# Kernel tuning notes

Measured on AMD Instinct MI355X. Metric: run time of the kernel, lower is better.

The kernel has to match this reference:

```python
import jax, jax.numpy as jnp
import numpy as np

N = 100000   # active voxels (stride=1 -> output coords == input coords)
C_IN = 64
C_OUT = 64
K3 = 27      # 3x3x3 kernel offsets
M = 40000    # rulebook pairs per kernel offset
EPS = 1e-5


def setup_inputs() -> dict:
    key = jax.random.key(0)
    k1, k2, k3, k4 = jax.random.split(key, 4)
    x = jax.random.normal(k1, (N, C_IN), dtype=jnp.float32)
    # conv weights per kernel offset: [K3, inc, outc]
    W = jax.random.normal(k2, (K3, C_IN, C_OUT), dtype=jnp.float32) * 0.05
    gamma = jnp.ones((C_OUT,), dtype=jnp.float32)
    beta = jnp.zeros((C_OUT,), dtype=jnp.float32)
    # rulebook: for each offset k, M (input_idx, output_idx) pairs
    in_idx = jax.random.randint(k3, (K3, M), 0, N, dtype=jnp.int32)
    out_idx = jax.random.randint(k4, (K3, M), 0, N, dtype=jnp.int32)
    return {"x": x, "W": W, "gamma": gamma, "beta": beta,
            "in_idx": in_idx, "out_idx": out_idx}


def reference(x, W, gamma, beta, in_idx, out_idx):
    n_out = x.shape[0]  # stride=1: output voxel set == input voxel set
    # gather: [K3, M, C_IN]
    feat = x[in_idx]
    # batched GEMM over kernel offsets: [K3, M, C_OUT]
    contrib = jnp.einsum('kmi,kio->kmo', feat, W)
    # scatter-add into output voxels
    out = jnp.zeros((n_out, W.shape[2]), dtype=x.dtype)
    out = out.at[out_idx.reshape(-1)].add(contrib.reshape(-1, W.shape[2]))
    # BatchNorm over active points (training-mode batch stats, biased var)
    mean = jnp.mean(out, axis=0)
    var = jnp.mean(jnp.square(out - mean), axis=0)
    y = (out - mean) * jax.lax.rsqrt(var + EPS) * gamma + beta
    # ReLU
    return jnp.maximum(y, 0.0)
```

## Files before the change

### kernel.cpp

```cpp
#include <hip/hip_runtime.h>


#define N_VOX   100000
#define NPAD    100096
#define K3      27
#define M_PAIRS 40000
#define NPAIRS  (K3 * M_PAIRS)
#define BN_EPS  1e-5f
#define NBINS   (K3 * NPAD)
#define AUXMAX  172032
#define AUXCAP  (AUXMAX - 1)
#define ZROW    (N_VOX + AUXMAX - 1)

#define OFF_WT     0u
#define OFF_STATS  221184u
#define OFF_CTRS   221696u
#define OFF_BT     221760u
#define OFF_NODE   11032128u
#define OFF_LIST   19672128u
#define OFF_XB     20360320u
#define OFF_BH     (OFF_XB + (size_t)N_VOX * 128u)
#define WS_NEED    ((size_t)OFF_XB + (size_t)(N_VOX + AUXMAX) * 128u)

#define NB_WT    432
#define NB_XB    3125
#define NB_BUILD 4219
#define GRID_IB  (NB_WT + NB_XB + 1 + NB_BUILD)

typedef __attribute__((ext_vector_type(8))) short bf16x8;
typedef __attribute__((ext_vector_type(4))) float f32x4;

__device__ __forceinline__ short f2bf(float f) {
  unsigned u = __builtin_bit_cast(unsigned, f);
  u += 0x7FFFu + ((u >> 16) & 1u);
  return (short)(u >> 16);
}
__device__ __forceinline__ float bf2f(short s) {
  unsigned u = ((unsigned)(unsigned short)s) << 16;
  return __builtin_bit_cast(float, u);
}

__global__ __launch_bounds__(256) void init_build_kernel(const float* __restrict__ W,
                                                         const float* __restrict__ x,
                                                         const int* __restrict__ in_idx,
                                                         const int* __restrict__ out_idx,
                                                         short* __restrict__ wt,
                                                         short* __restrict__ xb,
                                                         int* __restrict__ bh,
                                                         int2* __restrict__ node) {
  int b = blockIdx.x, t = threadIdx.x;
  if (b < NB_WT) {
    int id = b * 256 + t;
    int k = id >> 12, rem = id & 4095, c = rem >> 6, i = rem & 63;
    wt[id] = f2bf(W[(k << 12) + (i << 6) + c]);
  } else if (b < NB_WT + NB_XB) {
    int id = (b - NB_WT) * 256 + t;
    if (id < N_VOX * 8) {
      float4 lo = ((const float4*)x)[id * 2];
      float4 hi = ((const float4*)x)[id * 2 + 1];
      bf16x8 v;
      v[0] = f2bf(lo.x); v[1] = f2bf(lo.y); v[2] = f2bf(lo.z); v[3] = f2bf(lo.w);
      v[4] = f2bf(hi.x); v[5] = f2bf(hi.y); v[6] = f2bf(hi.z); v[7] = f2bf(hi.w);
      ((bf16x8*)xb)[id] = v;
    }
  } else if (b == NB_WT + NB_XB) {
    if (t < 8) {
      bf16x8 z = {0, 0, 0, 0, 0, 0, 0, 0};
      ((bf16x8*)(xb + (size_t)ZROW * 64))[t] = z;
    }
  } else {
    int id = (b - (NB_WT + NB_XB + 1)) * 256 + t;
    if (id < NPAIRS) {
      int k  = id / M_PAIRS;
      int in = in_idx[id];
      int o  = out_idx[id];
      int bb = k * NPAD + o;
      int old = atomicExch(&bh[bb], id);
      node[id] = make_int2(old, in);
    }
  }
}

__global__ __launch_bounds__(256) void compact_kernel(const int* __restrict__ bh,
                                                      const int2* __restrict__ node,
                                                      int* __restrict__ bt,
                                                      int* __restrict__ list,
                                                      int* __restrict__ ctrs) {
  __shared__ int l_cnt, l_base;
  int t = threadIdx.x;
  if (t == 0) l_cnt = 0;
  __syncthreads();
  int w = blockIdx.x * 256 + t;
  bool ok = (w < NBINS / 4);
  int4 h4 = ok ? ((const int4*)bh)[w] : make_int4(-1, -1, -1, -1);
  int hv[4] = {h4.x, h4.y, h4.z, h4.w};
  int gv[4], lp[4];
  int2 n0[4];
  #pragma unroll
  for (int s = 0; s < 4; ++s) {
    lp[s] = -1;
    if (hv[s] < 0) { gv[s] = ZROW; }
    else {
      n0[s] = node[hv[s]];
      if (n0[s].x < 0) gv[s] = n0[s].y;
      else             lp[s] = atomicAdd(&l_cnt, 1);
    }
  }
  __syncthreads();
  if (t == 0) l_base = (l_cnt > 0) ? atomicAdd(&ctrs[0], l_cnt) : 0;
  __syncthreads();
  #pragma unroll
  for (int s = 0; s < 4; ++s) {
    if (lp[s] >= 0) {
      int pos = l_base + lp[s];
      if (pos < AUXCAP) { list[pos] = hv[s]; gv[s] = N_VOX + pos; }
      else              { gv[s] = n0[s].y; }
    }
  }
  if (ok) {
    int b0 = w * 4;
    int k  = b0 / NPAD;
    int o0 = b0 - k * NPAD;
    #pragma unroll
    for (int s = 0; s < 4; ++s) bt[(size_t)(o0 + s) * K3 + k] = gv[s];
  }
}

__global__ __launch_bounds__(256) void fixup_kernel(short* __restrict__ xb,
                                                    const int* __restrict__ list,
                                                    const int2* __restrict__ node,
                                                    const int* __restrict__ ctrs) {
  int n = ctrs[0]; if (n > AUXCAP) n = AUXCAP;
  int wid  = (blockIdx.x * 256 + threadIdx.x) >> 6;
  int lane = threadIdx.x & 63;
  int nw   = gridDim.x * 4;
  for (int i = wid; i < n; i += nw) {
    int h = list[i];
    float acc = 0.f;
    while (h >= 0) {
      int2 nd = node[h];
      acc += bf2f(xb[(size_t)nd.y * 64 + lane]);
      h = nd.x;
    }
    xb[(size_t)(N_VOX + i) * 64 + lane] = f2bf(acc);
  }
}

__global__ __launch_bounds__(256, 6) void conv_out_kernel(const short* __restrict__ xb,
                                                          const short* __restrict__ wt,
                                                          const int* __restrict__ bt,
                                                          float* __restrict__ out,
                                                          float* __restrict__ stats) {
  __shared__ short lds[2 * 4096];
  __shared__ float ls[128];
  int t = threadIdx.x, wave = t >> 6, lane = t & 63;
  int g = lane >> 4, c0 = lane & 15, g8 = g * 8;
  int o = blockIdx.x * 64 + wave * 16 + c0;
  const int* bo = bt + (size_t)o * K3;

  int rb  = ((c0 * 128 + g * 16) ^ ((c0 & 7) << 4)) >> 1;
  int wb0 = ((t * 32) ^ (((t >> 2) & 7) << 4)) >> 1;
  if (t < 128) ls[t] = 0.f;

  f32x4 acc[4];
  #pragma unroll
  for (int n = 0; n < 4; ++n) { acc[n][0]=0.f; acc[n][1]=0.f; acc[n][2]=0.f; acc[n][3]=0.f; }

  bf16x8 s0w = *(const bf16x8*)(wt + t * 16);
  bf16x8 s1w = *(const bf16x8*)(wt + t * 16 + 8);
  int i0 = bo[0];
  const short* xr0 = xb + (size_t)i0 * 64;
  bf16x8 a0c = *(const bf16x8*)(xr0 + g8);
  bf16x8 a1c = *(const bf16x8*)(xr0 + 32 + g8);
  int i1 = bo[1];
  const short* xr1 = xb + (size_t)i1 * 64;
  bf16x8 a0n = *(const bf16x8*)(xr1 + g8);
  bf16x8 a1n = *(const bf16x8*)(xr1 + 32 + g8);
  *(bf16x8*)&lds[wb0]     = s0w;
  *(bf16x8*)&lds[wb0 ^ 8] = s1w;
  __syncthreads();

  int buf = 0;
  for (int k = 0; k < K3; ++k) {
    if (k + 1 < K3) {
      const short* wn = wt + (size_t)(k + 1) * 4096 + t * 16;
      s0w = *(const bf16x8*)(wn);
      s1w = *(const bf16x8*)(wn + 8);
    }
    int i2 = (k + 2 < K3) ? bo[k + 2] : ZROW;
    const short* xr2 = xb + (size_t)i2 * 64;
    bf16x8 a0m = *(const bf16x8*)(xr2 + g8);
    bf16x8 a1m = *(const bf16x8*)(xr2 + 32 + g8);

    const short* lb = lds + buf * 4096;
    #pragma unroll
    for (int n = 0; n < 4; ++n) {
      bf16x8 b0 = *(const bf16x8*)&lb[rb + n * 1024];
      bf16x8 b1 = *(const bf16x8*)&lb[(rb ^ 32) + n * 1024];
      acc[n] = __builtin_amdgcn_mfma_f32_16x16x32_bf16(a0c, b0, acc[n], 0, 0, 0);
      acc[n] = __builtin_amdgcn_mfma_f32_16x16x32_bf16(a1c, b1, acc[n], 0, 0, 0);
    }
    if (k + 1 < K3) {
      short* wd = lds + (buf ^ 1) * 4096;
      *(bf16x8*)&wd[wb0]     = s0w;
      *(bf16x8*)&wd[wb0 ^ 8] = s1w;
    }
    __syncthreads();
    a0c = a0n; a1c = a1n; a0n = a0m; a1n = a1m; buf ^= 1;
  }

  int orow = blockIdx.x * 64 + wave * 16 + (g << 2);
  #pragma unroll
  for (int j = 0; j < 4; ++j) {
    int r = orow + j;
    if (r < N_VOX) {
      float* op = out + (size_t)r * 64 + c0;
      op[0]  = acc[0][j];
      op[16] = acc[1][j];
      op[32] = acc[2][j];
      op[48] = acc[3][j];
    }
  }

  #pragma unroll
  for (int n = 0; n < 4; ++n) {
    float s = 0.f, q = 0.f;
    #pragma unroll
    for (int j = 0; j < 4; ++j) { float v = acc[n][j]; s += v; q += v * v; }
    atomicAdd(&ls[n * 16 + c0], s);
    atomicAdd(&ls[64 + n * 16 + c0], q);
  }
  __syncthreads();
  if (t < 128) unsafeAtomicAdd(&stats[t], ls[t]);
}

__global__ __launch_bounds__(256) void norm_kernel(float* __restrict__ out,
                                                   const float* __restrict__ stats,
                                                   const float* __restrict__ gamma,
                                                   const float* __restrict__ beta) {
  int i4 = blockIdx.x * 256 + threadIdx.x;
  if (i4 >= N_VOX * 16) return;
  const float invN = 1.0f / (float)N_VOX;
  float4 v = ((const float4*)out)[i4];
  int c0 = (i4 << 2) & 63;
  float r[4] = {v.x, v.y, v.z, v.w};
  #pragma unroll
  for (int j = 0; j < 4; ++j) {
    int c = c0 + j;
    float mean = stats[c] * invN;
    float ex2  = stats[64 + c] * invN;
    float var  = ex2 - mean * mean;
    float scale = gamma[c] * rsqrtf(var + BN_EPS);
    float shift = beta[c] - mean * scale;
    r[j] = fmaxf(r[j] * scale + shift, 0.0f);
  }
  v.x = r[0]; v.y = r[1]; v.z = r[2]; v.w = r[3];
  ((float4*)out)[i4] = v;
}

extern "C" void kernel_launch(void* const* d_in, const int* in_sizes, int n_in,
                              void* d_out, int out_size, void* d_ws, size_t ws_size,
                              hipStream_t stream) {
  const float* x      = (const float*)d_in[0];
  const float* W      = (const float*)d_in[1];
  const float* gamma  = (const float*)d_in[2];
  const float* beta   = (const float*)d_in[3];
  const int*   in_idx = (const int*)d_in[4];
  const int*   out_idx= (const int*)d_in[5];
  float* out = (float*)d_out;

  char* ws = (char*)d_ws;
  short* wt    = (short*)(ws + OFF_WT);
  float* stats = (float*)(ws + OFF_STATS);
  int*   ctrs  = (int*)(ws + OFF_CTRS);
  int*   bt    = (int*)(ws + OFF_BT);
  int2*  node  = (int2*)(ws + OFF_NODE);
  int*   list  = (int*)(ws + OFF_LIST);
  short* xb    = (short*)(ws + OFF_XB);
  int*   bh    = (int*)(ws + OFF_BH);

  hipMemsetAsync(ws + OFF_STATS, 0, OFF_BT - OFF_STATS, stream);
  hipMemsetAsync((void*)bh, 0xFF, (size_t)NBINS * 4, stream);

  init_build_kernel<<<GRID_IB, 256, 0, stream>>>(W, x, in_idx, out_idx,
                                                 wt, xb, bh, node);
  compact_kernel<<<(NBINS / 4 + 255) / 256, 256, 0, stream>>>(bh, node, bt, list, ctrs);
  fixup_kernel<<<4096, 256, 0, stream>>>(xb, list, node, ctrs);
  conv_out_kernel<<<NPAD / 64, 256, 0, stream>>>(xb, wt, bt, out, stats);
  norm_kernel<<<(N_VOX * 16 + 255) / 256, 256, 0, stream>>>(out, stats, gamma, beta);
}
```

Measured before the change: 255.9 us.

## Store two gather slots per bin and feed both rows directly into MFMA

```diff
diff --git a/kernel.cpp b/kernel.cpp
--- a/kernel.cpp
+++ b/kernel.cpp
@@ -8,19 +8,18 @@
 #define NPAIRS  (K3 * M_PAIRS)
 #define BN_EPS  1e-5f
 #define NBINS   (K3 * NPAD)
-#define AUXMAX  172032
+#define AUXMAX  49152
 #define AUXCAP  (AUXMAX - 1)
 #define ZROW    (N_VOX + AUXMAX - 1)
 
 #define OFF_WT     0u
 #define OFF_STATS  221184u
 #define OFF_CTRS   221696u
-#define OFF_BT     221760u
-#define OFF_NODE   11032128u
-#define OFF_LIST   19672128u
-#define OFF_XB     20360320u
-#define OFF_BH     (OFF_XB + (size_t)N_VOX * 128u)
-#define WS_NEED    ((size_t)OFF_XB + (size_t)(N_VOX + AUXMAX) * 128u)
+#define OFF_BG2    221760u
+#define OFF_NODE   21842496u
+#define OFF_LIST   30482496u
+#define OFF_XB     30679104u
+#define OFF_BH     49770560u
 
 #define NB_WT    432
 #define NB_XB    3125
@@ -83,7 +82,7 @@
 
 __global__ __launch_bounds__(256) void compact_kernel(const int* __restrict__ bh,
                                                       const int2* __restrict__ node,
-                                                      int* __restrict__ bt,
+                                                      int2* __restrict__ bg2,
                                                       int* __restrict__ list,
                                                       int* __restrict__ ctrs) {
   __shared__ int l_cnt, l_base;
@@ -94,16 +93,18 @@
   bool ok = (w < NBINS / 4);
   int4 h4 = ok ? ((const int4*)bh)[w] : make_int4(-1, -1, -1, -1);
   int hv[4] = {h4.x, h4.y, h4.z, h4.w};
-  int gv[4], lp[4];
-  int2 n0[4];
+  int g0[4], g1[4], lp[4];
   #pragma unroll
   for (int s = 0; s < 4; ++s) {
-    lp[s] = -1;
-    if (hv[s] < 0) { gv[s] = ZROW; }
-    else {
-      n0[s] = node[hv[s]];
-      if (n0[s].x < 0) gv[s] = n0[s].y;
-      else             lp[s] = atomicAdd(&l_cnt, 1);
+    lp[s] = -1; g0[s] = ZROW; g1[s] = ZROW;
+    if (hv[s] >= 0) {
+      int2 n0 = node[hv[s]];
+      g0[s] = n0.y;
+      if (n0.x >= 0) {
+        int2 n1 = node[n0.x];
+        g1[s] = n1.y;
+        if (n1.x >= 0) lp[s] = atomicAdd(&l_cnt, 1);
+      }
     }
   }
   __syncthreads();
@@ -113,16 +114,12 @@
   for (int s = 0; s < 4; ++s) {
     if (lp[s] >= 0) {
       int pos = l_base + lp[s];
-      if (pos < AUXCAP) { list[pos] = hv[s]; gv[s] = N_VOX + pos; }
-      else              { gv[s] = n0[s].y; }
+      if (pos < AUXCAP) { list[pos] = hv[s]; g0[s] = N_VOX + pos; g1[s] = ZROW; }
     }
   }
   if (ok) {
-    int b0 = w * 4;
-    int k  = b0 / NPAD;
-    int o0 = b0 - k * NPAD;
-    #pragma unroll
-    for (int s = 0; s < 4; ++s) bt[(size_t)(o0 + s) * K3 + k] = gv[s];
+    ((int4*)bg2)[w * 2]     = make_int4(g0[0], g1[0], g0[1], g1[1]);
+    ((int4*)bg2)[w * 2 + 1] = make_int4(g0[2], g1[2], g0[3], g1[3]);
   }
 }
 
@@ -146,36 +143,41 @@
   }
 }
 
-__global__ __launch_bounds__(256, 6) void conv_out_kernel(const short* __restrict__ xb,
-                                                          const short* __restrict__ wt,
-                                                          const int* __restrict__ bt,
-                                                          float* __restrict__ out,
-                                                          float* __restrict__ stats) {
+#define LOADROW(d0, d1, idx)                                    \
+  { const short* _p = xb + (size_t)(idx) * 64;                  \
+    d0 = *(const bf16x8*)(_p + g8);                             \
+    d1 = *(const bf16x8*)(_p + 32 + g8); }
+
+__global__ __launch_bounds__(256) void conv_out_kernel(const short* __restrict__ xb,
+                                                       const short* __restrict__ wt,
+                                                       const int2* __restrict__ bg,
+                                                       float* __restrict__ out,
+                                                       float* __restrict__ stats) {
   __shared__ short lds[2 * 4096];
   __shared__ float ls[128];
   int t = threadIdx.x, wave = t >> 6, lane = t & 63;
   int g = lane >> 4, c0 = lane & 15, g8 = g * 8;
-  int o = blockIdx.x * 64 + wave * 16 + c0;
-  const int* bo = bt + (size_t)o * K3;
+  int o0 = blockIdx.x * 128 + wave * 32 + c0;
+  int o1 = o0 + 16;
 
   int rb  = ((c0 * 128 + g * 16) ^ ((c0 & 7) << 4)) >> 1;
   int wb0 = ((t * 32) ^ (((t >> 2) & 7) << 4)) >> 1;
   if (t < 128) ls[t] = 0.f;
 
-  f32x4 acc[4];
-  #pragma unroll
-  for (int n = 0; n < 4; ++n) { acc[n][0]=0.f; acc[n][1]=0.f; acc[n][2]=0.f; acc[n][3]=0.f; }
+  f32x4 acc0[4], acc1[4];
+  #pragma unroll
+  for (int n = 0; n < 4; ++n) {
+    acc0[n][0]=0.f; acc0[n][1]=0.f; acc0[n][2]=0.f; acc0[n][3]=0.f;
+    acc1[n][0]=0.f; acc1[n][1]=0.f; acc1[n][2]=0.f; acc1[n][3]=0.f;
+  }
 
   bf16x8 s0w = *(const bf16x8*)(wt + t * 16);
   bf16x8 s1w = *(const bf16x8*)(wt + t * 16 + 8);
-  int i0 = bo[0];
-  const short* xr0 = xb + (size_t)i0 * 64;
-  bf16x8 a0c = *(const bf16x8*)(xr0 + g8);
-  bf16x8 a1c = *(const bf16x8*)(xr0 + 32 + g8);
-  int i1 = bo[1];
-  const short* xr1 = xb + (size_t)i1 * 64;
-  bf16x8 a0n = *(const bf16x8*)(xr1 + g8);
-  bf16x8 a1n = *(const bf16x8*)(xr1 + 32 + g8);
+  int2 gac = bg[o0], gbc = bg[o1];
+  bf16x8 ap0c, ap1c, as0c, as1c, bp0c, bp1c, bs0c, bs1c;
+  LOADROW(ap0c, ap1c, gac.x); LOADROW(as0c, as1c, gac.y);
+  LOADROW(bp0c, bp1c, gbc.x); LOADROW(bs0c, bs1c, gbc.y);
+  int2 gan = bg[NPAD + o0], gbn = bg[NPAD + o1];
   *(bf16x8*)&lds[wb0]     = s0w;
   *(bf16x8*)&lds[wb0 ^ 8] = s1w;
   __syncthreads();
@@ -187,18 +189,27 @@
       s0w = *(const bf16x8*)(wn);
       s1w = *(const bf16x8*)(wn + 8);
     }
-    int i2 = (k + 2 < K3) ? bo[k + 2] : ZROW;
-    const short* xr2 = xb + (size_t)i2 * 64;
-    bf16x8 a0m = *(const bf16x8*)(xr2 + g8);
-    bf16x8 a1m = *(const bf16x8*)(xr2 + 32 + g8);
-
+    bf16x8 ap0n, ap1n, as0n, as1n, bp0n, bp1n, bs0n, bs1n;
+    LOADROW(ap0n, ap1n, gan.x); LOADROW(as0n, as1n, gan.y);
+    LOADROW(bp0n, bp1n, gbn.x); LOADROW(bs0n, bs1n, gbn.y);
+    int2 gann = make_int2(ZROW, ZROW), gbnn = make_int2(ZROW, ZROW);
+    if (k + 2 < K3) {
+      gann = bg[(size_t)(k + 2) * NPAD + o0];
+      gbnn = bg[(size_t)(k + 2) * NPAD + o1];
+    }
     const short* lb = lds + buf * 4096;
     #pragma unroll
     for (int n = 0; n < 4; ++n) {
       bf16x8 b0 = *(const bf16x8*)&lb[rb + n * 1024];
       bf16x8 b1 = *(const bf16x8*)&lb[(rb ^ 32) + n * 1024];
-      acc[n] = __builtin_amdgcn_mfma_f32_16x16x32_bf16(a0c, b0, acc[n], 0, 0, 0);
-      acc[n] = __builtin_amdgcn_mfma_f32_16x16x32_bf16(a1c, b1, acc[n], 0, 0, 0);
+      acc0[n] = __builtin_amdgcn_mfma_f32_16x16x32_bf16(ap0c, b0, acc0[n], 0, 0, 0);
+      acc0[n] = __builtin_amdgcn_mfma_f32_16x16x32_bf16(ap1c, b1, acc0[n], 0, 0, 0);
+      acc0[n] = __builtin_amdgcn_mfma_f32_16x16x32_bf16(as0c, b0, acc0[n], 0, 0, 0);
+      acc0[n] = __builtin_amdgcn_mfma_f32_16x16x32_bf16(as1c, b1, acc0[n], 0, 0, 0);
+      acc1[n] = __builtin_amdgcn_mfma_f32_16x16x32_bf16(bp0c, b0, acc1[n], 0, 0, 0);
+      acc1[n] = __builtin_amdgcn_mfma_f32_16x16x32_bf16(bp1c, b1, acc1[n], 0, 0, 0);
+      acc1[n] = __builtin_amdgcn_mfma_f32_16x16x32_bf16(bs0c, b0, acc1[n], 0, 0, 0);
+      acc1[n] = __builtin_amdgcn_mfma_f32_16x16x32_bf16(bs1c, b1, acc1[n], 0, 0, 0);
     }
     if (k + 1 < K3) {
       short* wd = lds + (buf ^ 1) * 4096;
@@ -206,19 +217,22 @@
       *(bf16x8*)&wd[wb0 ^ 8] = s1w;
     }
     __syncthreads();
-    a0c = a0n; a1c = a1n; a0n = a0m; a1n = a1m; buf ^= 1;
-  }
-
-  int orow = blockIdx.x * 64 + wave * 16 + (g << 2);
+    ap0c = ap0n; ap1c = ap1n; as0c = as0n; as1c = as1n;
+    bp0c = bp0n; bp1c = bp1n; bs0c = bs0n; bs1c = bs1n;
+    gan = gann; gbn = gbnn; buf ^= 1;
+  }
+
+  int orow = blockIdx.x * 128 + wave * 32 + (g << 2);
   #pragma unroll
   for (int j = 0; j < 4; ++j) {
-    int r = orow + j;
-    if (r < N_VOX) {
-      float* op = out + (size_t)r * 64 + c0;
-      op[0]  = acc[0][j];
-      op[16] = acc[1][j];
-      op[32] = acc[2][j];
-      op[48] = acc[3][j];
+    int r0 = orow + j, r1 = orow + 16 + j;
+    if (r0 < N_VOX) {
+      float* op = out + (size_t)r0 * 64 + c0;
+      op[0] = acc0[0][j]; op[16] = acc0[1][j]; op[32] = acc0[2][j]; op[48] = acc0[3][j];
+    }
+    if (r1 < N_VOX) {
+      float* op = out + (size_t)r1 * 64 + c0;
+      op[0] = acc1[0][j]; op[16] = acc1[1][j]; op[32] = acc1[2][j]; op[48] = acc1[3][j];
     }
   }
 
@@ -226,7 +240,10 @@
   for (int n = 0; n < 4; ++n) {
     float s = 0.f, q = 0.f;
     #pragma unroll
-    for (int j = 0; j < 4; ++j) { float v = acc[n][j]; s += v; q += v * v; }
+    for (int j = 0; j < 4; ++j) {
+      float v0 = acc0[n][j], v1 = acc1[n][j];
+      s += v0 + v1; q += v0 * v0 + v1 * v1;
+    }
     atomicAdd(&ls[n * 16 + c0], s);
     atomicAdd(&ls[64 + n * 16 + c0], q);
   }
@@ -273,19 +290,19 @@
   short* wt    = (short*)(ws + OFF_WT);
   float* stats = (float*)(ws + OFF_STATS);
   int*   ctrs  = (int*)(ws + OFF_CTRS);
-  int*   bt    = (int*)(ws + OFF_BT);
+  int2*  bg2   = (int2*)(ws + OFF_BG2);
   int2*  node  = (int2*)(ws + OFF_NODE);
   int*   list  = (int*)(ws + OFF_LIST);
   short* xb    = (short*)(ws + OFF_XB);
   int*   bh    = (int*)(ws + OFF_BH);
 
-  hipMemsetAsync(ws + OFF_STATS, 0, OFF_BT - OFF_STATS, stream);
+  hipMemsetAsync(ws + OFF_STATS, 0, OFF_BG2 - OFF_STATS, stream);
   hipMemsetAsync((void*)bh, 0xFF, (size_t)NBINS * 4, stream);
 
   init_build_kernel<<<GRID_IB, 256, 0, stream>>>(W, x, in_idx, out_idx,
                                                  wt, xb, bh, node);
-  compact_kernel<<<(NBINS / 4 + 255) / 256, 256, 0, stream>>>(bh, node, bt, list, ctrs);
-  fixup_kernel<<<4096, 256, 0, stream>>>(xb, list, node, ctrs);
-  conv_out_kernel<<<NPAD / 64, 256, 0, stream>>>(xb, wt, bt, out, stats);
+  compact_kernel<<<(NBINS / 4 + 255) / 256, 256, 0, stream>>>(bh, node, bg2, list, ctrs);
+  fixup_kernel<<<1024, 256, 0, stream>>>(xb, list, node, ctrs);
+  conv_out_kernel<<<NPAD / 128, 256, 0, stream>>>(xb, wt, bg2, out, stats);
   norm_kernel<<<(N_VOX * 16 + 255) / 256, 256, 0, stream>>>(out, stats, gamma, beta);
 }
```

After: 216.3 us. 1.18x faster.
